# Optimization experiments

Measured on AMD Instinct MI355X. Metric: run time of the kernel, lower is better.

The kernel has to match this reference:

```python
import jax, jax.numpy as jnp
import numpy as np

BN_EPS = 1e-3  # Keras BatchNormalization default epsilon


def setup_inputs() -> dict:
    key = jax.random.key(0)
    ks = jax.random.split(key, 16)
    B, N, M = 4, 16384, 4096
    C1, C2 = 128, 256
    mlp = [256, 128]
    cin = C2 + C1
    inp = {
        "xyz1": jax.random.normal(ks[0], (B, N, 3), dtype=jnp.float32),
        "xyz2": jax.random.normal(ks[1], (B, M, 3), dtype=jnp.float32),
        "points1": jax.random.normal(ks[2], (B, N, C1), dtype=jnp.float32),
        "points2": jax.random.normal(ks[3], (B, M, C2), dtype=jnp.float32),
    }
    k = 4
    for i, cout in enumerate(mlp):
        inp[f"w{i}"] = jax.random.normal(ks[k], (cin, cout), dtype=jnp.float32) * (1.0 / np.sqrt(cin)); k += 1
        inp[f"g{i}"] = jnp.ones((cout,), dtype=jnp.float32) + 0.1 * jax.random.normal(ks[k], (cout,), dtype=jnp.float32); k += 1
        inp[f"b{i}"] = 0.1 * jax.random.normal(ks[k], (cout,), dtype=jnp.float32); k += 1
        inp[f"m{i}"] = 0.1 * jax.random.normal(ks[k], (cout,), dtype=jnp.float32); k += 1
        inp[f"v{i}"] = 0.5 + jax.random.uniform(ks[k], (cout,), dtype=jnp.float32); k += 1
        cin = cout
    return inp


def _three_nn(xyz1, xyz2):
    # squared pairwise distances [B,N,M] via ||a||^2 + ||b||^2 - 2ab
    n1 = jnp.sum(xyz1 * xyz1, axis=-1)                      # [B,N]
    n2 = jnp.sum(xyz2 * xyz2, axis=-1)                      # [B,M]
    d2 = n1[:, :, None] + n2[:, None, :] - 2.0 * jnp.einsum("bnc,bmc->bnm", xyz1, xyz2)
    d2 = jnp.maximum(d2, 0.0)
    neg, idx = jax.lax.top_k(-d2, 3)                        # 3 smallest distances
    return -neg, idx                                        # dist [B,N,3], idx [B,N,3]


def reference(xyz1, xyz2, points1, points2,
              w0, g0, b0, m0, v0, w1, g1, b1, m1, v1):
    dist, idx = _three_nn(xyz1, xyz2)
    dist = jnp.maximum(dist, 1e-10)
    inv = 1.0 / dist                                        # [B,N,3]
    weight = inv / jnp.sum(inv, axis=2, keepdims=True)      # [B,N,3]
    # three_interpolate: irregular gather + weighted sum
    gathered = jax.vmap(lambda p, i: p[i])(points2, idx)    # [B,N,3,C2]
    interp = jnp.einsum("bnk,bnkc->bnc", weight, gathered)  # [B,N,C2]
    x = jnp.concatenate([interp, points1], axis=2)          # [B,N,C2+C1]
    # 1x1 Conv2D (no bias) + BN(inference) + ReLU stack
    for w, g, b, m, v in ((w0, g0, b0, m0, v0), (w1, g1, b1, m1, v1)):
        x = jnp.einsum("bnc,cd->bnd", x, w)
        x = (x - m) * (g * jax.lax.rsqrt(v + BN_EPS)) + b
        x = jax.nn.relu(x)
    return x
```

## Files before the change

### kernel.cpp

```cpp
#include <hip/hip_runtime.h>
#include <hip/hip_bf16.h>

typedef __bf16 bf16x8 __attribute__((ext_vector_type(8)));
typedef float  f32x4  __attribute__((ext_vector_type(4)));
typedef unsigned short ushort_t;
typedef unsigned int   uint_t;

__device__ __forceinline__ ushort_t f2bf(float f) {
    union { float f; uint_t u; } v; v.f = f;
    uint_t r = v.u + 0x7fffu + ((v.u >> 16) & 1u);
    return (ushort_t)(r >> 16);
}

__device__ __forceinline__ void async_copy16(const void* g, void* l) {
    __builtin_amdgcn_global_load_lds(
        (const __attribute__((address_space(1))) unsigned int*)g,
        (__attribute__((address_space(3))) unsigned int*)l, 16, 0, 0);
}

#define BATCH 4
#define NPTS  16384
#define MPTS  4096
#define C1    128
#define C2    256
#define NCHUNK 4
#define CHUNK  (MPTS / NCHUNK)

__global__ __launch_bounds__(256) void prep_kernel(
    const float* __restrict__ w0, const float* __restrict__ w1,
    const float* __restrict__ g0, const float* __restrict__ b0,
    const float* __restrict__ m0, const float* __restrict__ v0,
    const float* __restrict__ g1, const float* __restrict__ b1,
    const float* __restrict__ m1, const float* __restrict__ v1,
    ushort_t* __restrict__ wt0, ushort_t* __restrict__ wt1,
    float* __restrict__ sc0, float* __restrict__ sh0,
    float* __restrict__ sc1, float* __restrict__ sh1) {
    int i = blockIdx.x * 256 + threadIdx.x;
    if (i < 256 * 384) {
        int n = i / 384, k = i % 384;
        wt0[i] = f2bf(w0[k * 256 + n]);
    }
    if (i < 128 * 256) {
        int n = i / 256, k = i % 256;
        wt1[i] = f2bf(w1[k * 128 + n]);
    }
    if (i < 256) { float s = g0[i] * rsqrtf(v0[i] + 1e-3f); sc0[i] = s; sh0[i] = b0[i] - m0[i] * s; }
    if (i < 128) { float s = g1[i] * rsqrtf(v1[i] + 1e-3f); sc1[i] = s; sh1[i] = b1[i] - m1[i] * s; }
}

__global__ __launch_bounds__(256) void knn_partial(
    const float* __restrict__ xyz1, const float* __restrict__ xyz2,
    float* __restrict__ pd, int* __restrict__ pi) {
    __shared__ __align__(16) float sx[CHUNK], sy[CHUNK], sz[CHUNK], sw[CHUNK];
    const int t  = threadIdx.x;
    const int qb = blockIdx.x;
    const int c  = blockIdx.y;
    const int b  = blockIdx.z;
#pragma unroll
    for (int j = 0; j < CHUNK / 256; j++) {
        const int m = j * 256 + t;
        const float* g = xyz2 + ((long)b * MPTS + c * CHUNK + m) * 3;
        const float x = g[0], y = g[1], z = g[2];
        sx[m] = x; sy[m] = y; sz[m] = z; sw[m] = x * x + y * y + z * z;
    }
    __syncthreads();
    const int n = qb * 256 + t;
    const long base = ((long)b * NPTS + n) * 3;
    const float qx = xyz1[base], qy = xyz1[base + 1], qz = xyz1[base + 2];
    const float nx = -2.f * qx, ny = -2.f * qy, nz = -2.f * qz;
    float d0 = 3.4e38f, d1 = 3.4e38f, d2 = 3.4e38f;
    int   i0 = 0, i1 = 0, i2 = 0;
    const int mb = c * CHUNK;
    for (int g = 0; g < CHUNK; g += 4) {
        const float4 X = *(const float4*)&sx[g];
        const float4 Y = *(const float4*)&sy[g];
        const float4 Z = *(const float4*)&sz[g];
        const float4 W = *(const float4*)&sw[g];
        const float xs[4] = {X.x, X.y, X.z, X.w};
        const float ys[4] = {Y.x, Y.y, Y.z, Y.w};
        const float zs[4] = {Z.x, Z.y, Z.z, Z.w};
        const float ws[4] = {W.x, W.y, W.z, W.w};
#pragma unroll
        for (int j = 0; j < 4; j++) {
            const float s = fmaf(xs[j], nx, fmaf(ys[j], ny, fmaf(zs[j], nz, ws[j])));
            if (__ballot(s < d2)) {
                const int m = mb + g + j;
                const bool c0 = s < d0, c1 = s < d1, c2 = s < d2;
                const float nd2 = c1 ? d1 : (c2 ? s : d2);
                const int   ni2 = c1 ? i1 : (c2 ? m : i2);
                const float nd1 = c0 ? d0 : (c1 ? s : d1);
                const int   ni1 = c0 ? i0 : (c1 ? m : i1);
                d0 = c0 ? s : d0; i0 = c0 ? m : i0;
                d1 = nd1; i1 = ni1; d2 = nd2; i2 = ni2;
            }
        }
    }
    const long po = ((long)c * (BATCH * NPTS) + (long)b * NPTS + n) * 3;
    pd[po] = d0; pd[po + 1] = d1; pd[po + 2] = d2;
    pi[po] = i0; pi[po + 1] = i1; pi[po + 2] = i2;
}

__global__ __launch_bounds__(256) void knn_merge(
    const float* __restrict__ xyz1,
    const float* __restrict__ pd, const int* __restrict__ pi,
    int* __restrict__ idx, float* __restrict__ wgt) {
    const long n = blockIdx.x * 256 + threadIdx.x;
    float d0 = 3.4e38f, d1 = 3.4e38f, d2 = 3.4e38f;
    int   i0 = 0, i1 = 0, i2 = 0;
#pragma unroll
    for (int c = 0; c < NCHUNK; c++) {
        const long po = ((long)c * (BATCH * NPTS) + n) * 3;
#pragma unroll
        for (int k = 0; k < 3; k++) {
            const float d = pd[po + k];
            const int   m = pi[po + k];
            const bool c0 = d < d0, c1 = d < d1, c2 = d < d2;
            const float nd2 = c1 ? d1 : (c2 ? d : d2);
            const int   ni2 = c1 ? i1 : (c2 ? m : i2);
            const float nd1 = c0 ? d0 : (c1 ? d : d1);
            const int   ni1 = c0 ? i0 : (c1 ? m : i1);
            d0 = c0 ? d : d0;  i0 = c0 ? m : i0;
            d1 = nd1; i1 = ni1; d2 = nd2; i2 = ni2;
        }
    }
    const float qx = xyz1[n * 3], qy = xyz1[n * 3 + 1], qz = xyz1[n * 3 + 2];
    const float qn = qx * qx + qy * qy + qz * qz;
    d0 = fmaxf(d0 + qn, 1e-10f);
    d1 = fmaxf(d1 + qn, 1e-10f);
    d2 = fmaxf(d2 + qn, 1e-10f);
    const float w0 = 1.f / d0, w1 = 1.f / d1, w2 = 1.f / d2;
    const float rs = 1.f / (w0 + w1 + w2);
    const long o = n * 3;
    idx[o] = i0; idx[o + 1] = i1; idx[o + 2] = i2;
    wgt[o] = w0 * rs; wgt[o + 1] = w1 * rs; wgt[o + 2] = w2 * rs;
}

__global__ __launch_bounds__(256) void interp_kernel(
    const float* __restrict__ points1, const float* __restrict__ points2,
    const int* __restrict__ idx, const float* __restrict__ wgt,
    ushort_t* __restrict__ x0) {
    const int wave = (blockIdx.x * 256 + threadIdx.x) >> 6;
    const int lane = threadIdx.x & 63;
    const int b = wave >> 14;
    const int n = wave & 16383;
    const long o = (long)wave * 3;
    int i0 = idx[o], i1 = idx[o + 1], i2 = idx[o + 2];
    i0 = min(max(i0, 0), MPTS - 1);
    i1 = min(max(i1, 0), MPTS - 1);
    i2 = min(max(i2, 0), MPTS - 1);
    const float w0 = wgt[o], w1 = wgt[o + 1], w2 = wgt[o + 2];
    const float4* p0 = (const float4*)(points2 + ((long)b * MPTS + i0) * C2);
    const float4* p1 = (const float4*)(points2 + ((long)b * MPTS + i1) * C2);
    const float4* p2 = (const float4*)(points2 + ((long)b * MPTS + i2) * C2);
    float4 a = p0[lane], bb = p1[lane], c = p2[lane];
    ushort4 u;
    u.x = f2bf(w0 * a.x + w1 * bb.x + w2 * c.x);
    u.y = f2bf(w0 * a.y + w1 * bb.y + w2 * c.y);
    u.z = f2bf(w0 * a.z + w1 * bb.z + w2 * c.z);
    u.w = f2bf(w0 * a.w + w1 * bb.w + w2 * c.w);
    ((ushort4*)(x0 + (long)wave * 384))[lane] = u;
    const float2* q = (const float2*)(points1 + ((long)b * NPTS + n) * C1);
    float2 t = q[lane];
    uint_t packed = (uint_t)f2bf(t.x) | ((uint_t)f2bf(t.y) << 16);
    ((uint_t*)(x0 + (long)wave * 384 + 256))[lane] = packed;
}

template <int K, bool OUT_BF16>
__global__ __launch_bounds__(256) void gemm_bn_relu(
    const ushort_t* __restrict__ A,
    const ushort_t* __restrict__ Bt,
    const float* __restrict__ scale, const float* __restrict__ shift,
    void* __restrict__ outp, int ldout) {
    __shared__ ushort_t lds[8192];
    ushort_t* ldsA = lds;
    ushort_t* ldsB = lds + 4096;
    const int tid  = threadIdx.x;
    const int wv   = tid >> 6;
    const int lane = tid & 63;
    const int q    = lane >> 4, l16 = lane & 15;
    const int rowBase = blockIdx.x * 128;
    const int colBase = blockIdx.y * 128;
    const int wrow = (wv & 1) * 64, wcol = (wv >> 1) * 64;
    f32x4 acc[4][4] = {};

    for (int kk = 0; kk < K; kk += 32) {
#pragma unroll
        for (int ch = 0; ch < 2; ch++) {
            const int linear = ch * 4096 + tid * 16;
            const int row = linear >> 6;
            const int brow = linear & 63;
            const char* ga = (const char*)A + ((long)(rowBase + row) * K + kk) * 2 + brow;
            async_copy16(ga, (char*)ldsA + ch * 4096 + wv * 1024);
            const char* gb = (const char*)Bt + ((long)(colBase + row) * K + kk) * 2 + brow;
            async_copy16(gb, (char*)ldsB + ch * 4096 + wv * 1024);
        }
        __syncthreads();
        bf16x8 af[4], bfr[4];
#pragma unroll
        for (int t = 0; t < 4; t++) {
            const int r = wrow + t * 16 + l16;
            af[t]  = *(const bf16x8*)((const char*)ldsA + r * 64 + q * 16);
            const int c = wcol + t * 16 + l16;
            bfr[t] = *(const bf16x8*)((const char*)ldsB + c * 64 + q * 16);
        }
#pragma unroll
        for (int tr = 0; tr < 4; tr++)
#pragma unroll
            for (int tc = 0; tc < 4; tc++)
                acc[tr][tc] = __builtin_amdgcn_mfma_f32_16x16x32_bf16(af[tr], bfr[tc], acc[tr][tc], 0, 0, 0);
        __syncthreads();
    }
#pragma unroll
    for (int tc = 0; tc < 4; tc++) {
        const int col = colBase + wcol + tc * 16 + l16;
        const float sc = scale[col], sh = shift[col];
#pragma unroll
        for (int tr = 0; tr < 4; tr++) {
            const int row0 = rowBase + wrow + tr * 16 + q * 4;
#pragma unroll
            for (int r = 0; r < 4; r++) {
                float v = acc[tr][tc][r];
                v = fmaxf(v * sc + sh, 0.0f);
                const long off = (long)(row0 + r) * ldout + col;
                if (OUT_BF16) ((ushort_t*)outp)[off] = f2bf(v);
                else          ((float*)outp)[off]    = v;
            }
        }
    }
}

extern "C" void kernel_launch(void* const* d_in, const int* in_sizes, int n_in,
                              void* d_out, int out_size, void* d_ws, size_t ws_size,
                              hipStream_t stream) {
    const float* xyz1    = (const float*)d_in[0];
    const float* xyz2    = (const float*)d_in[1];
    const float* points1 = (const float*)d_in[2];
    const float* points2 = (const float*)d_in[3];
    const float* w0 = (const float*)d_in[4];
    const float* g0 = (const float*)d_in[5];
    const float* b0 = (const float*)d_in[6];
    const float* m0 = (const float*)d_in[7];
    const float* v0 = (const float*)d_in[8];
    const float* w1 = (const float*)d_in[9];
    const float* g1 = (const float*)d_in[10];
    const float* b1 = (const float*)d_in[11];
    const float* m1 = (const float*)d_in[12];
    const float* v1 = (const float*)d_in[13];

    char* ws = (char*)d_ws;
    int*      idx = (int*)ws;
    float*    wgt = (float*)(ws + 786432);
    ushort_t* wt0 = (ushort_t*)(ws + 1572864);
    ushort_t* wt1 = (ushort_t*)(ws + 1769472);
    float*    sc0 = (float*)(ws + 1835008);
    float*    sh0 = sc0 + 256;
    float*    sc1 = sh0 + 256;
    float*    sh1 = sc1 + 128;
    ushort_t* x0  = (ushort_t*)(ws + 2097152);
    ushort_t* y1  = (ushort_t*)(ws + 2097152 + 50331648);
    float* pd = (float*)(ws + 2097152);
    int*   pi = (int*)(ws + 2097152 + 6291456);

    prep_kernel<<<384, 256, 0, stream>>>(w0, w1, g0, b0, m0, v0, g1, b1, m1, v1,
                                         wt0, wt1, sc0, sh0, sc1, sh1);
    knn_partial<<<dim3(NPTS / 256, NCHUNK, BATCH), 256, 0, stream>>>(xyz1, xyz2, pd, pi);
    knn_merge<<<(BATCH * NPTS) / 256, 256, 0, stream>>>(xyz1, pd, pi, idx, wgt);
    interp_kernel<<<(BATCH * NPTS) / 4, 256, 0, stream>>>(points1, points2, idx, wgt, x0);
    gemm_bn_relu<384, true ><<<dim3((BATCH * NPTS) / 128, 2), 256, 0, stream>>>(
        x0, wt0, sc0, sh0, (void*)y1, 256);
    gemm_bn_relu<256, false><<<dim3((BATCH * NPTS) / 128, 1), 256, 0, stream>>>(
        y1, wt1, sc1, sh1, d_out, 128);
}
```

Before: 262.9 us.

## Fuse two MLP GEMMs via LDS intermediate and split KNN into branchless two-pass search

The two GEMM+BN+ReLU kernels become one kernel over 64-row tiles. The bf16 hidden activations stay in LDS, so the global round-trip for the 256-wide intermediate is gone. Separately, the KNN partial pass now finds the three smallest distances branchlessly with fmin/fmed3, then makes a second pass to recover indices by equality matching. The costs are that the fused kernel re-reads A for each half and uses smaller tiles with larger LDS, and the KNN does twice the distance computation.

```diff
diff --git a/kernel.cpp b/kernel.cpp
--- a/kernel.cpp
+++ b/kernel.cpp
@@ -51,7 +51,7 @@
 __global__ __launch_bounds__(256) void knn_partial(
     const float* __restrict__ xyz1, const float* __restrict__ xyz2,
     float* __restrict__ pd, int* __restrict__ pi) {
-    __shared__ __align__(16) float sx[CHUNK], sy[CHUNK], sz[CHUNK], sw[CHUNK];
+    __shared__ __align__(16) float sx[CHUNK], sy_[CHUNK], sz[CHUNK], sw[CHUNK];
     const int t  = threadIdx.x;
     const int qb = blockIdx.x;
     const int c  = blockIdx.y;
@@ -61,7 +61,7 @@
         const int m = j * 256 + t;
         const float* g = xyz2 + ((long)b * MPTS + c * CHUNK + m) * 3;
         const float x = g[0], y = g[1], z = g[2];
-        sx[m] = x; sy[m] = y; sz[m] = z; sw[m] = x * x + y * y + z * z;
+        sx[m] = x; sy_[m] = y; sz[m] = z; sw[m] = x * x + y * y + z * z;
     }
     __syncthreads();
     const int n = qb * 256 + t;
@@ -69,11 +69,10 @@
     const float qx = xyz1[base], qy = xyz1[base + 1], qz = xyz1[base + 2];
     const float nx = -2.f * qx, ny = -2.f * qy, nz = -2.f * qz;
     float d0 = 3.4e38f, d1 = 3.4e38f, d2 = 3.4e38f;
-    int   i0 = 0, i1 = 0, i2 = 0;
-    const int mb = c * CHUNK;
+
     for (int g = 0; g < CHUNK; g += 4) {
         const float4 X = *(const float4*)&sx[g];
-        const float4 Y = *(const float4*)&sy[g];
+        const float4 Y = *(const float4*)&sy_[g];
         const float4 Z = *(const float4*)&sz[g];
         const float4 W = *(const float4*)&sw[g];
         const float xs[4] = {X.x, X.y, X.z, X.w};
@@ -83,15 +82,36 @@
 #pragma unroll
         for (int j = 0; j < 4; j++) {
             const float s = fmaf(xs[j], nx, fmaf(ys[j], ny, fmaf(zs[j], nz, ws[j])));
-            if (__ballot(s < d2)) {
+            const float n0 = fminf(d0, s);
+            const float n1 = __builtin_amdgcn_fmed3f(d0, d1, s);
+            const float n2 = __builtin_amdgcn_fmed3f(d1, d2, s);
+            d0 = n0; d1 = n1; d2 = n2;
+        }
+    }
+
+    int i0 = 0, i1 = 0, i2 = 0;
+    bool f0 = false, f1 = false, f2 = false;
+    const int mb = c * CHUNK;
+    for (int g = 0; g < CHUNK; g += 4) {
+        const float4 X = *(const float4*)&sx[g];
+        const float4 Y = *(const float4*)&sy_[g];
+        const float4 Z = *(const float4*)&sz[g];
+        const float4 W = *(const float4*)&sw[g];
+        const float xs[4] = {X.x, X.y, X.z, X.w};
+        const float ys[4] = {Y.x, Y.y, Y.z, Y.w};
+        const float zs[4] = {Z.x, Z.y, Z.z, Z.w};
+        const float ws[4] = {W.x, W.y, W.z, W.w};
+#pragma unroll
+        for (int j = 0; j < 4; j++) {
+            const float s = fmaf(xs[j], nx, fmaf(ys[j], ny, fmaf(zs[j], nz, ws[j])));
+            if (__ballot(s <= d2)) {
                 const int m = mb + g + j;
-                const bool c0 = s < d0, c1 = s < d1, c2 = s < d2;
-                const float nd2 = c1 ? d1 : (c2 ? s : d2);
-                const int   ni2 = c1 ? i1 : (c2 ? m : i2);
-                const float nd1 = c0 ? d0 : (c1 ? s : d1);
-                const int   ni1 = c0 ? i0 : (c1 ? m : i1);
-                d0 = c0 ? s : d0; i0 = c0 ? m : i0;
-                d1 = nd1; i1 = ni1; d2 = nd2; i2 = ni2;
+                const bool m0 = (s == d0) && !f0;
+                const bool m1 = (s == d1) && !f1 && !m0;
+                const bool m2 = (s == d2) && !f2 && !m1 && !m0;
+                i0 = m0 ? m : i0; f0 = f0 || m0;
+                i1 = m1 ? m : i1; f1 = f1 || m1;
+                i2 = m2 ? m : i2; f2 = f2 || m2;
             }
         }
     }
@@ -165,65 +185,107 @@
     ((uint_t*)(x0 + (long)wave * 384 + 256))[lane] = packed;
 }
 
-template <int K, bool OUT_BF16>
-__global__ __launch_bounds__(256) void gemm_bn_relu(
+__global__ __launch_bounds__(256) void mlp_fused(
     const ushort_t* __restrict__ A,
-    const ushort_t* __restrict__ Bt,
-    const float* __restrict__ scale, const float* __restrict__ shift,
-    void* __restrict__ outp, int ldout) {
-    __shared__ ushort_t lds[8192];
-    ushort_t* ldsA = lds;
-    ushort_t* ldsB = lds + 4096;
-    const int tid  = threadIdx.x;
-    const int wv   = tid >> 6;
-    const int lane = tid & 63;
-    const int q    = lane >> 4, l16 = lane & 15;
-    const int rowBase = blockIdx.x * 128;
-    const int colBase = blockIdx.y * 128;
-    const int wrow = (wv & 1) * 64, wcol = (wv >> 1) * 64;
-    f32x4 acc[4][4] = {};
-
-    for (int kk = 0; kk < K; kk += 32) {
+    const ushort_t* __restrict__ Bt0,
+    const ushort_t* __restrict__ Bt1,
+    const float* __restrict__ sc0, const float* __restrict__ sh0,
+    const float* __restrict__ sc1, const float* __restrict__ sh1,
+    float* __restrict__ outp) {
+    __shared__ ushort_t sA[2048];
+    __shared__ ushort_t sB[4096];
+    __shared__ ushort_t sy[64 * 264];
+    const int tid = threadIdx.x;
+    const int wv = tid >> 6, lane = tid & 63;
+    const int q = lane >> 4, l16 = lane & 15;
+    const int rowBase = blockIdx.x * 64;
+    const int wrow = (wv & 1) * 32;
+    const int wcol = (wv >> 1) * 64;
+
+#pragma unroll 1
+    for (int H = 0; H < 2; H++) {
+        f32x4 acc[2][4] = {};
+        for (int kk = 0; kk < 384; kk += 32) {
+            {
+                const int linear = tid * 16;
+                const int row = linear >> 6, brow = linear & 63;
+                const char* ga = (const char*)A + ((long)(rowBase + row) * 384 + kk) * 2 + brow;
+                async_copy16(ga, (char*)sA + wv * 1024);
+            }
+#pragma unroll
+            for (int ch = 0; ch < 2; ch++) {
+                const int linear = ch * 4096 + tid * 16;
+                const int row = linear >> 6, brow = linear & 63;
+                const char* gb = (const char*)Bt0 + ((long)(H * 128 + row) * 384 + kk) * 2 + brow;
+                async_copy16(gb, (char*)sB + ch * 4096 + wv * 1024);
+            }
+            __syncthreads();
+            bf16x8 af[2], bfr[4];
+#pragma unroll
+            for (int t = 0; t < 2; t++)
+                af[t] = *(const bf16x8*)((const char*)sA + (wrow + t * 16 + l16) * 64 + q * 16);
+#pragma unroll
+            for (int t = 0; t < 4; t++)
+                bfr[t] = *(const bf16x8*)((const char*)sB + (wcol + t * 16 + l16) * 64 + q * 16);
+#pragma unroll
+            for (int tr = 0; tr < 2; tr++)
+#pragma unroll
+                for (int tc = 0; tc < 4; tc++)
+                    acc[tr][tc] = __builtin_amdgcn_mfma_f32_16x16x32_bf16(af[tr], bfr[tc], acc[tr][tc], 0, 0, 0);
+            __syncthreads();
+        }
+#pragma unroll
+        for (int tc = 0; tc < 4; tc++) {
+            const int ycol = H * 128 + wcol + tc * 16 + l16;
+            const float sc = sc0[ycol], sh = sh0[ycol];
+#pragma unroll
+            for (int tr = 0; tr < 2; tr++) {
+                const int row0 = wrow + tr * 16 + q * 4;
+#pragma unroll
+                for (int r = 0; r < 4; r++) {
+                    const float v = fmaxf(acc[tr][tc][r] * sc + sh, 0.f);
+                    sy[(row0 + r) * 264 + ycol] = f2bf(v);
+                }
+            }
+        }
+    }
+    __syncthreads();
+
+    f32x4 acc2[2][4] = {};
+    for (int kk = 0; kk < 256; kk += 32) {
 #pragma unroll
         for (int ch = 0; ch < 2; ch++) {
             const int linear = ch * 4096 + tid * 16;
-            const int row = linear >> 6;
-            const int brow = linear & 63;
-            const char* ga = (const char*)A + ((long)(rowBase + row) * K + kk) * 2 + brow;
-            async_copy16(ga, (char*)ldsA + ch * 4096 + wv * 1024);
-            const char* gb = (const char*)Bt + ((long)(colBase + row) * K + kk) * 2 + brow;
-            async_copy16(gb, (char*)ldsB + ch * 4096 + wv * 1024);
+            const int row = linear >> 6, brow = linear & 63;
+            const char* gb = (const char*)Bt1 + ((long)row * 256 + kk) * 2 + brow;
+            async_copy16(gb, (char*)sB + ch * 4096 + wv * 1024);
         }
         __syncthreads();
-        bf16x8 af[4], bfr[4];
-#pragma unroll
-        for (int t = 0; t < 4; t++) {
-            const int r = wrow + t * 16 + l16;
-            af[t]  = *(const bf16x8*)((const char*)ldsA + r * 64 + q * 16);
-            const int c = wcol + t * 16 + l16;
-            bfr[t] = *(const bf16x8*)((const char*)ldsB + c * 64 + q * 16);
-        }
-#pragma unroll
-        for (int tr = 0; tr < 4; tr++)
+        bf16x8 af2[2], bf2[4];
+#pragma unroll
+        for (int t = 0; t < 2; t++)
+            af2[t] = *(const bf16x8*)((const char*)sy + (wrow + t * 16 + l16) * 528 + kk * 2 + q * 16);
+#pragma unroll
+        for (int t = 0; t < 4; t++)
+            bf2[t] = *(const bf16x8*)((const char*)sB + (wcol + t * 16 + l16) * 64 + q * 16);
+#pragma unroll
+        for (int tr = 0; tr < 2; tr++)
 #pragma unroll
             for (int tc = 0; tc < 4; tc++)
-                acc[tr][tc] = __builtin_amdgcn_mfma_f32_16x16x32_bf16(af[tr], bfr[tc], acc[tr][tc], 0, 0, 0);
+                acc2[tr][tc] = __builtin_amdgcn_mfma_f32_16x16x32_bf16(af2[tr], bf2[tc], acc2[tr][tc], 0, 0, 0);
         __syncthreads();
     }
 #pragma unroll
     for (int tc = 0; tc < 4; tc++) {
-        const int col = colBase + wcol + tc * 16 + l16;
-        const float sc = scale[col], sh = shift[col];
-#pragma unroll
-        for (int tr = 0; tr < 4; tr++) {
+        const int col = wcol + tc * 16 + l16;
+        const float sc = sc1[col], sh = sh1[col];
+#pragma unroll
+        for (int tr = 0; tr < 2; tr++) {
             const int row0 = rowBase + wrow + tr * 16 + q * 4;
 #pragma unroll
             for (int r = 0; r < 4; r++) {
-                float v = acc[tr][tc][r];
-                v = fmaxf(v * sc + sh, 0.0f);
-                const long off = (long)(row0 + r) * ldout + col;
-                if (OUT_BF16) ((ushort_t*)outp)[off] = f2bf(v);
-                else          ((float*)outp)[off]    = v;
+                const float v = fmaxf(acc2[tr][tc][r] * sc + sh, 0.f);
+                outp[(long)(row0 + r) * 128 + col] = v;
             }
         }
     }
@@ -257,7 +319,6 @@
     float*    sc1 = sh0 + 256;
     float*    sh1 = sc1 + 128;
     ushort_t* x0  = (ushort_t*)(ws + 2097152);
-    ushort_t* y1  = (ushort_t*)(ws + 2097152 + 50331648);
     float* pd = (float*)(ws + 2097152);
     int*   pi = (int*)(ws + 2097152 + 6291456);
 
@@ -266,8 +327,6 @@
     knn_partial<<<dim3(NPTS / 256, NCHUNK, BATCH), 256, 0, stream>>>(xyz1, xyz2, pd, pi);
     knn_merge<<<(BATCH * NPTS) / 256, 256, 0, stream>>>(xyz1, pd, pi, idx, wgt);
     interp_kernel<<<(BATCH * NPTS) / 4, 256, 0, stream>>>(points1, points2, idx, wgt, x0);
-    gemm_bn_relu<384, true ><<<dim3((BATCH * NPTS) / 128, 2), 256, 0, stream>>>(
-        x0, wt0, sc0, sh0, (void*)y1, 256);
-    gemm_bn_relu<256, false><<<dim3((BATCH * NPTS) / 128, 1), 256, 0, stream>>>(
-        y1, wt1, sc1, sh1, d_out, 128);
-}
+    mlp_fused<<<(BATCH * NPTS) / 64, 256, 0, stream>>>(
+        x0, wt0, wt1, sc0, sh0, sc1, sh1, (float*)d_out);
+}
```

Result: slower. 280.6 us (+6.7%).
